# Optimization experiments

Hardware: AMD Instinct MI355X
Metric: run time of the kernel (lower is better)

The kernel has to match this reference:

```python
import jax, jax.numpy as jnp
import numpy as np

# Scaled-up constants (GRID_SIZE=96)
AFFINE_HIDDEN_DIM = 128
ATTENTION_DIM = 256
EMBEDDING_DIM = 512
MAX_CONTRAST = 1.8
RANGE_SIZE = 4
NUM_RANGE_BLOCKS = 13824   # (96//4)**3
NUM_DOMAIN_BLOCKS = 1728   # (96//8)**3
SOFTMAX_TEMPERATURE = 0.25


def setup_inputs() -> dict:
    key = jax.random.key(0)
    ks = jax.random.split(key, 17)
    E, A, H = EMBEDDING_DIM, ATTENTION_DIM, AFFINE_HIDDEN_DIM
    NR, ND = NUM_RANGE_BLOCKS, NUM_DOMAIN_BLOCKS
    s_lin = 1.0 / np.sqrt(E)  # torch Linear default init scale
    return {
        "pooled_domains": jax.random.normal(ks[0], (ND, RANGE_SIZE, RANGE_SIZE, RANGE_SIZE), jnp.float32),
        "range_latents": jax.random.normal(ks[1], (NR, E), jnp.float32),
        "domain_latents": jax.random.normal(ks[2], (ND, E), jnp.float32),
        "range_positional": jax.random.normal(ks[3], (NR, E), jnp.float32),
        "domain_positional": jax.random.normal(ks[4], (ND, E), jnp.float32),
        "W_rproj": jax.random.normal(ks[5], (E, A), jnp.float32) * s_lin,
        "b_rproj": jax.random.normal(ks[6], (A,), jnp.float32) * s_lin,
        "W_dproj": jax.random.normal(ks[7], (E, A), jnp.float32) * s_lin,
        "b_dproj": jax.random.normal(ks[8], (A,), jnp.float32) * s_lin,
        "W_rcon": jax.random.normal(ks[9], (E, H), jnp.float32) * s_lin,
        "b_rcon": jax.random.normal(ks[10], (H,), jnp.float32) * s_lin,
        "W_dcon": jax.random.normal(ks[11], (E, H), jnp.float32) * s_lin,
        "b_dcon": jax.random.normal(ks[12], (H,), jnp.float32) * s_lin,
        "W_roff": jax.random.normal(ks[13], (E, H), jnp.float32) * s_lin,
        "b_roff": jax.random.normal(ks[14], (H,), jnp.float32) * s_lin,
        "W_doff": jax.random.normal(ks[15], (E, H), jnp.float32) * s_lin,
        "b_doff": jax.random.normal(ks[16], (H,), jnp.float32) * s_lin,
    }


def reference(pooled_domains, range_latents, domain_latents,
              range_positional, domain_positional,
              W_rproj, b_rproj, W_dproj, b_dproj,
              W_rcon, b_rcon, W_dcon, b_dcon,
              W_roff, b_roff, W_doff, b_doff):
    range_base = range_latents + range_positional      # [NR, E]
    domain_base = domain_latents + domain_positional   # [ND, E]

    range_repr = range_base @ W_rproj + b_rproj        # [NR, A]
    domain_repr = domain_base @ W_dproj + b_dproj      # [ND, A]

    inv_sqrt_h = 1.0 / np.sqrt(AFFINE_HIDDEN_DIM).astype(np.float32)
    range_con = range_base @ W_rcon + b_rcon           # [NR, H]
    domain_con = domain_base @ W_dcon + b_dcon         # [ND, H]
    contrast = jnp.tanh((range_con @ domain_con.T) * inv_sqrt_h) * MAX_CONTRAST  # [NR, ND]

    range_off = range_base @ W_roff + b_roff
    domain_off = domain_base @ W_doff + b_doff
    offset = jnp.tanh((range_off @ domain_off.T) * inv_sqrt_h)  # [NR, ND]

    scale = 1.0 / (np.sqrt(ATTENTION_DIM).astype(np.float32) * SOFTMAX_TEMPERATURE)
    logits = (range_repr @ domain_repr.T) * scale      # [NR, ND]
    weights = jax.nn.softmax(logits, axis=-1)          # [NR, ND]

    domain_flat = pooled_domains.reshape(NUM_DOMAIN_BLOCKS, -1)   # [ND, 64]
    scaled_domains = (weights * contrast) @ domain_flat           # [NR, 64]
    offset_effective = jnp.sum(weights * offset, axis=1, keepdims=True)  # [NR, 1]
    decoded = (scaled_domains + offset_effective).reshape(-1, RANGE_SIZE, RANGE_SIZE, RANGE_SIZE)
    return decoded
```

## Files before the change

kernel.cpp:

```cpp
#include <hip/hip_runtime.h>
#include <stdint.h>

#define NRB 13824
#define NDB 1728
#define EDIM 512
#define SPLIT 18
#define DPB (NDB/SPLIT)
#define TILES (DPB/32)

typedef __attribute__((ext_vector_type(8))) _Float16 h8;
typedef __attribute__((ext_vector_type(4))) float f4;
typedef __attribute__((ext_vector_type(4))) unsigned short us4;

typedef __attribute__((address_space(3))) void lds_void;
typedef const __attribute__((address_space(1))) void gbl_void;

#define MFMA(a,b,c) __builtin_amdgcn_mfma_f32_16x16x32_f16(a,b,c,0,0,0)

static __device__ __forceinline__ ushort f2h(float f){
  union { _Float16 h; ushort u; } cv;
  cv.h = (_Float16)f;
  return cv.u;
}

static __device__ __forceinline__ float tanh_fast(float x){
  float ax = __builtin_fabsf(x);
  float t = __builtin_amdgcn_exp2f(ax * -2.8853900817779268f);
  float r = (1.0f - t) * __builtin_amdgcn_rcpf(1.0f + t);
  return __builtin_copysignf(r, x);
}

__global__ void prep_kernel(
    const float* __restrict__ pooled,
    const float* __restrict__ rlat, const float* __restrict__ dlat,
    const float* __restrict__ rpos, const float* __restrict__ dpos,
    const float* __restrict__ Wrp, const float* __restrict__ brp,
    const float* __restrict__ Wdp, const float* __restrict__ bdp,
    const float* __restrict__ Wrc, const float* __restrict__ brc,
    const float* __restrict__ Wdc, const float* __restrict__ bdc,
    const float* __restrict__ Wro, const float* __restrict__ bro,
    const float* __restrict__ Wdo2, const float* __restrict__ bdo2,
    ushort* __restrict__ rb, ushort* __restrict__ db,
    ushort* __restrict__ Wr_t, ushort* __restrict__ Wd_t,
    float* __restrict__ br_c, float* __restrict__ bd_c,
    ushort* __restrict__ dflt)
{
  const int NRE = NRB*EDIM, NDE = NDB*EDIM;
  int i0 = blockIdx.x*blockDim.x + threadIdx.x;
  int stride = gridDim.x*blockDim.x;
  for (int i=i0; i<NRE; i+=stride) rb[i] = f2h(rlat[i]+rpos[i]);
  for (int i=i0; i<NDE; i+=stride) db[i] = f2h(dlat[i]+dpos[i]);
  for (int i=i0; i<512*512; i+=stride){
    int n = i>>9, k = i&511;
    float vr = (n<256) ? Wrp[k*256+n] : ((n<384) ? Wrc[k*128+(n-256)] : Wro[k*128+(n-384)]);
    float vd = (n<256) ? Wdp[k*256+n] : ((n<384) ? Wdc[k*128+(n-256)] : Wdo2[k*128+(n-384)]);
    Wr_t[i] = f2h(vr); Wd_t[i] = f2h(vd);
  }
  for (int i=i0; i<512; i+=stride){
    br_c[i] = (i<256) ? brp[i] : ((i<384) ? brc[i-256] : bro[i-384]);
    bd_c[i] = (i<256) ? bdp[i] : ((i<384) ? bdc[i-256] : bdo2[i-384]);
  }
  for (int i=i0; i<64*NDB; i+=stride){
    int c = i/NDB, d = i - c*NDB;
    dflt[i] = f2h(pooled[d*64+c]);
  }
}

__global__ __launch_bounds__(256) void gemm_feats(
    const ushort* __restrict__ A,
    const ushort* __restrict__ Bt,
    const float* __restrict__ bias,
    ushort* __restrict__ C,
    int M)
{
  __shared__ ushort As[128*32];
  __shared__ ushort Bs[128*32];
  const int tid = threadIdx.x;
  const int lane = tid & 63;
  const int wave = tid >> 6;
  const int l15 = lane & 15;
  const int lhi = lane >> 4;
  const int row0 = blockIdx.x * 128;
  const int col0 = blockIdx.y * 128;
  const int wr = (wave>>1)*64;
  const int wc = (wave&1)*64;

  f4 acc[4][4] = {};
  char* Ab = (char*)As; char* Bb = (char*)Bs;

  for (int k0=0; k0<EDIM; k0+=32){
    __syncthreads();
    #pragma unroll
    for (int c=0;c<2;c++){
      int L = (tid + c*256)*16;
      int r = L>>6;
      int kb = L&63;
      int kbs = kb ^ ((r&3)<<4);
      int ra = row0 + r; if (ra > M-1) ra = M-1;
      const ushort* srcA = A + (size_t)ra*EDIM + k0 + (kbs>>1);
      const ushort* srcB = Bt + (size_t)(col0+r)*EDIM + k0 + (kbs>>1);
      __builtin_amdgcn_global_load_lds((gbl_void*)srcA, (lds_void*)(Ab + L), 16, 0, 0);
      __builtin_amdgcn_global_load_lds((gbl_void*)srcB, (lds_void*)(Bb + L), 16, 0, 0);
    }
    __syncthreads();
    h8 af[4], bf[4];
    #pragma unroll
    for (int i=0;i<4;i++){
      int rowa = wr + i*16 + l15;
      af[i] = *(const h8*)(Ab + (((rowa*64) + lhi*16) ^ ((rowa&3)<<4)));
      int rowb = wc + i*16 + l15;
      bf[i] = *(const h8*)(Bb + (((rowb*64) + lhi*16) ^ ((rowb&3)<<4)));
    }
    #pragma unroll
    for (int i=0;i<4;i++){
      #pragma unroll
      for (int j=0;j<4;j++){
        acc[i][j] = MFMA(af[i], bf[j], acc[i][j]);
      }
    }
  }

  #pragma unroll
  for (int j=0;j<4;j++){
    int col = col0 + wc + j*16 + l15;
    float bv = bias[col];
    #pragma unroll
    for (int i=0;i<4;i++){
      #pragma unroll
      for (int r=0;r<4;r++){
        int row = row0 + wr + i*16 + lhi*4 + r;
        if (row < M) C[(size_t)row*EDIM + col] = f2h(acc[i][j][r] + bv);
      }
    }
  }
}

__global__ __launch_bounds__(512, 2) void attn_kernel(
    const ushort* __restrict__ rfeat,
    const ushort* __restrict__ dfeat,
    const ushort* __restrict__ dflt,
    ushort* __restrict__ accbuf,
    float* __restrict__ mlbuf)
{
  __shared__ ushort DF[DPB*512];
  __shared__ ushort PT[8][16*32];

  const int tid  = threadIdx.x;
  const int wave = tid >> 6;
  const int lane = tid & 63;
  const int l15  = lane & 15;
  const int lhi  = lane >> 4;
  const int wrow = blockIdx.x*128 + wave*16;
  const int by   = blockIdx.y;
  const int dbase = by * DPB;

  constexpr float CL = 0.25f * 1.4426950408889634f;
  constexpr float CH = 0.08838834764831845f;

  char* DFb = (char*)DF;
  char* PTb = (char*)PT[wave];

  #pragma unroll
  for (int c=0;c<12;c++){
    int id = tid + c*512;
    int dom = id >> 6;
    h8 v = *(const h8*)(dfeat + (size_t)(dbase+dom)*EDIM + (id&63)*8);
    *(h8*)(DFb + ((id*16) ^ ((dom&7)<<4))) = v;
  }

  h8 q[16];
  {
    const ushort* qr = rfeat + (size_t)(wrow + l15)*EDIM + lhi*8;
    #pragma unroll
    for (int c=0;c<16;c++) q[c] = *(const h8*)(qr + c*32);
  }

  f4 acc[4] = {};
  float m = -1e30f, lsum = 0.f, offa = 0.f;
  const int sb = (lane & 48) + ((lane >> 4) << 2);

  __syncthreads();

  for (int t=0; t<TILES; ++t){
    const int d0 = dbase + t*32;
    const int dloc = t*32;

    f4 SL[2] = {}, SC[2] = {}, SO[2] = {};
    #pragma unroll
    for (int ct=0; ct<2; ++ct){
      const int dom = dloc + ct*16 + l15;
      const int swz = (dom&7)<<4;
      const int base = dom*1024 + lhi*16;
      #pragma unroll
      for (int c=0;c<8;c++){
        h8 b = *(const h8*)(DFb + ((base + c*64) ^ swz));
        SL[ct] = MFMA(b, q[c], SL[ct]);
      }
      #pragma unroll
      for (int c=8;c<12;c++){
        h8 b = *(const h8*)(DFb + ((base + c*64) ^ swz));
        SC[ct] = MFMA(b, q[c], SC[ct]);
      }
      #pragma unroll
      for (int c=12;c<16;c++){
        h8 b = *(const h8*)(DFb + ((base + c*64) ^ swz));
        SO[ct] = MFMA(b, q[c], SO[ct]);
      }
    }

    float lm = fmaxf(
        fmaxf(fmaxf(SL[0][0],SL[0][1]), fmaxf(SL[0][2],SL[0][3])),
        fmaxf(fmaxf(SL[1][0],SL[1][1]), fmaxf(SL[1][2],SL[1][3]))) * CL;
    lm = fmaxf(lm, __shfl_xor(lm, 16, 64));
    lm = fmaxf(lm, __shfl_xor(lm, 32, 64));
    float mn = fmaxf(m, lm);
    float al = __builtin_amdgcn_exp2f(m - mn);
    m = mn;
    lsum *= al; offa *= al;

    us4 w0, w1;
    #pragma unroll
    for (int r=0;r<4;r++){
      float p0 = __builtin_amdgcn_exp2f(SL[0][r]*CL - mn);
      float p1 = __builtin_amdgcn_exp2f(SL[1][r]*CL - mn);
      lsum += p0 + p1;
      float c0 = tanh_fast(SC[0][r]*CH)*1.8f;
      float c1 = tanh_fast(SC[1][r]*CH)*1.8f;
      float o0 = tanh_fast(SO[0][r]*CH);
      float o1 = tanh_fast(SO[1][r]*CH);
      offa += p0*o0 + p1*o1;
      w0[r] = f2h(p0*c0);
      w1[r] = f2h(p1*c1);
    }
    {
      const int wbase = l15*64;
      const int xs = (l15&3)<<4;
      *(us4*)(PTb + ((wbase + lhi*8) ^ xs))      = w0;
      *(us4*)(PTb + ((wbase + 32 + lhi*8) ^ xs)) = w1;
    }

    __builtin_amdgcn_sched_barrier(0);

    {
      float alr[4];
      #pragma unroll
      for (int r=0;r<4;r++) alr[r] = __shfl(al, sb + r, 64);
      #pragma unroll
      for (int nt=0; nt<4; nt++){
        acc[nt][0]*=alr[0]; acc[nt][1]*=alr[1];
        acc[nt][2]*=alr[2]; acc[nt][3]*=alr[3];
      }
      h8 pa = *(const h8*)(PTb + ((l15*64 + lhi*16) ^ ((l15&3)<<4)));
      #pragma unroll
      for (int nt=0; nt<4; nt++){
        int n = nt*16 + l15;
        h8 vb = *(const h8*)(dflt + (size_t)n*NDB + d0 + lhi*8);
        acc[nt] = MFMA(pa, vb, acc[nt]);
      }
    }

    __builtin_amdgcn_sched_barrier(0);
  }

  float ls = lsum, oa = offa;
  ls += __shfl_xor(ls, 16, 64); ls += __shfl_xor(ls, 32, 64);
  oa += __shfl_xor(oa, 16, 64); oa += __shfl_xor(oa, 32, 64);

  #pragma unroll
  for (int r=0;r<4;r++){
    int row = wrow + lhi*4 + r;
    size_t base = ((size_t)by*NRB + row)*64;
    #pragma unroll
    for (int nt=0; nt<4; nt++){
      accbuf[base + nt*16 + l15] = f2h(acc[nt][r]);
    }
  }
  if (lane < 16){
    size_t mo = ((size_t)by*NRB + wrow + l15)*4;
    mlbuf[mo+0] = m;
    mlbuf[mo+1] = ls;
    mlbuf[mo+2] = oa;
  }
}

__global__ __launch_bounds__(256) void combine_kernel(
    const ushort* __restrict__ accbuf,
    const float* __restrict__ mlbuf,
    float* __restrict__ out)
{
  __shared__ float wS[64][SPLIT];
  __shared__ float c0S[64], iTS[64];
  const int rb = blockIdx.x;
  const int tid = threadIdx.x;

  if (tid < 64){
    int row = rb*64 + tid;
    float M = -1e30f;
    float m[SPLIT], l[SPLIT], o[SPLIT];
    #pragma unroll
    for (int s=0;s<SPLIT;s++){
      size_t off = ((size_t)s*NRB + row)*4;
      m[s]=mlbuf[off]; l[s]=mlbuf[off+1]; o[s]=mlbuf[off+2];
      M = fmaxf(M, m[s]);
    }
    float T=0.f, C=0.f;
    #pragma unroll
    for (int s=0;s<SPLIT;s++){
      float w = __builtin_amdgcn_exp2f(m[s]-M);
      wS[tid][s]=w; T += l[s]*w; C += o[s]*w;
    }
    c0S[tid]=C; iTS[tid]=1.0f/T;
  }
  __syncthreads();

  const int row_l = tid>>2;
  const int cb = (tid&3)*16;
  const int row = rb*64 + row_l;
  float res[16] = {};
  #pragma unroll
  for (int s=0;s<SPLIT;s++){
    float w = wS[row_l][s];
    const ushort* ap = accbuf + ((size_t)s*NRB + row)*64 + cb;
    h8 v0 = *(const h8*)(ap);
    h8 v1 = *(const h8*)(ap + 8);
    #pragma unroll
    for (int j=0;j<8;j++){
      res[j]   += (float)v0[j]*w;
      res[j+8] += (float)v1[j]*w;
    }
  }
  float C = c0S[row_l], iT = iTS[row_l];
  #pragma unroll
  for (int j=0;j<16;j++) out[(size_t)row*64 + cb + j] = (res[j]+C)*iT;
}

extern "C" void kernel_launch(void* const* d_in, const int* in_sizes, int n_in,
                              void* d_out, int out_size, void* d_ws, size_t ws_size,
                              hipStream_t stream) {
  const float* pooled = (const float*)d_in[0];
  const float* rlat   = (const float*)d_in[1];
  const float* dlat   = (const float*)d_in[2];
  const float* rpos   = (const float*)d_in[3];
  const float* dpos   = (const float*)d_in[4];
  const float* Wrp    = (const float*)d_in[5];
  const float* brp    = (const float*)d_in[6];
  const float* Wdp    = (const float*)d_in[7];
  const float* bdp    = (const float*)d_in[8];
  const float* Wrc    = (const float*)d_in[9];
  const float* brc    = (const float*)d_in[10];
  const float* Wdc    = (const float*)d_in[11];
  const float* bdc    = (const float*)d_in[12];
  const float* Wro    = (const float*)d_in[13];
  const float* bro    = (const float*)d_in[14];
  const float* Wdo2   = (const float*)d_in[15];
  const float* bdo2   = (const float*)d_in[16];

  char* ws = (char*)d_ws;
  size_t off = 0;
  ushort* rb    = (ushort*)(ws + off); off += (size_t)NRB*EDIM*2;
  ushort* db    = (ushort*)(ws + off); off += (size_t)NDB*EDIM*2;
  ushort* Wr_t  = (ushort*)(ws + off); off += (size_t)512*512*2;
  ushort* Wd_t  = (ushort*)(ws + off); off += (size_t)512*512*2;
  float*  br_c  = (float*)(ws + off);  off += 512*4;
  float*  bd_c  = (float*)(ws + off);  off += 512*4;
  ushort* rfeat = (ushort*)(ws + off); off += (size_t)NRB*EDIM*2;
  ushort* dfeat = (ushort*)(ws + off); off += (size_t)NDB*EDIM*2;
  ushort* dflt  = (ushort*)(ws + off); off += (size_t)64*NDB*2;
  ushort* accb  = (ushort*)(ws + off); off += (size_t)SPLIT*NRB*64*2;
  float*  mlb   = (float*)(ws + off);  off += (size_t)SPLIT*NRB*4*4;

  prep_kernel<<<2048, 256, 0, stream>>>(pooled, rlat, dlat, rpos, dpos,
      Wrp, brp, Wdp, bdp, Wrc, brc, Wdc, bdc, Wro, bro, Wdo2, bdo2,
      rb, db, Wr_t, Wd_t, br_c, bd_c, dflt);

  gemm_feats<<<dim3(108,4), 256, 0, stream>>>(rb, Wr_t, br_c, rfeat, NRB);
  gemm_feats<<<dim3(14,4),  256, 0, stream>>>(db, Wd_t, bd_c, dfeat, NDB);

  attn_kernel<<<dim3(108, SPLIT), 512, 0, stream>>>(rfeat, dfeat, dflt, accb, mlb);
  combine_kernel<<<216, 256, 0, stream>>>(accb, mlb, (float*)d_out);
}
```

Baseline: 150.6 us.

## Process two query row-groups per wave to reuse LDS domain tiles

Each wave now handles two 16-row query groups (256 rows per block) instead of one, so every domain-feature fragment read from LDS and every dflt global load feeds two sets of MFMAs. The grid is halved in x, which halves the per-block LDS fill of domain features overall. The cost is double the query registers (32 h8) and accumulators per wave, which under launch_bounds(512,2) may cause spills or lower occupancy, and only 972 blocks remain to spread across the CUs.

```diff
diff --git a/kernel.cpp b/kernel.cpp
--- a/kernel.cpp
+++ b/kernel.cpp
@@ -143,22 +143,22 @@
     float* __restrict__ mlbuf)
 {
   __shared__ ushort DF[DPB*512];
-  __shared__ ushort PT[8][16*32];
+  __shared__ ushort PT[8][2][16*32];
 
   const int tid  = threadIdx.x;
   const int wave = tid >> 6;
   const int lane = tid & 63;
   const int l15  = lane & 15;
   const int lhi  = lane >> 4;
-  const int wrow = blockIdx.x*128 + wave*16;
   const int by   = blockIdx.y;
   const int dbase = by * DPB;
+  const int wrow0 = blockIdx.x*256 + wave*16;
+  const int wrow1 = wrow0 + 128;
 
   constexpr float CL = 0.25f * 1.4426950408889634f;
   constexpr float CH = 0.08838834764831845f;
 
   char* DFb = (char*)DF;
-  char* PTb = (char*)PT[wave];
 
   #pragma unroll
   for (int c=0;c<12;c++){
@@ -168,15 +168,16 @@
     *(h8*)(DFb + ((id*16) ^ ((dom&7)<<4))) = v;
   }
 
-  h8 q[16];
-  {
-    const ushort* qr = rfeat + (size_t)(wrow + l15)*EDIM + lhi*8;
-    #pragma unroll
-    for (int c=0;c<16;c++) q[c] = *(const h8*)(qr + c*32);
-  }
-
-  f4 acc[4] = {};
-  float m = -1e30f, lsum = 0.f, offa = 0.f;
+  h8 q[2][16];
+  #pragma unroll
+  for (int g=0; g<2; g++){
+    const ushort* qr = rfeat + (size_t)((g ? wrow1 : wrow0) + l15)*EDIM + lhi*8;
+    #pragma unroll
+    for (int c=0;c<16;c++) q[g][c] = *(const h8*)(qr + c*32);
+  }
+
+  f4 acc[2][4] = {};
+  float m[2] = {-1e30f, -1e30f}, lsum[2] = {0.f,0.f}, offa[2] = {0.f,0.f};
   const int sb = (lane & 48) + ((lane >> 4) << 2);
 
   __syncthreads();
@@ -185,101 +186,120 @@
     const int d0 = dbase + t*32;
     const int dloc = t*32;
 
-    f4 SL[2] = {}, SC[2] = {}, SO[2] = {};
-    #pragma unroll
-    for (int ct=0; ct<2; ++ct){
-      const int dom = dloc + ct*16 + l15;
-      const int swz = (dom&7)<<4;
-      const int base = dom*1024 + lhi*16;
-      #pragma unroll
-      for (int c=0;c<8;c++){
-        h8 b = *(const h8*)(DFb + ((base + c*64) ^ swz));
-        SL[ct] = MFMA(b, q[c], SL[ct]);
-      }
-      #pragma unroll
-      for (int c=8;c<12;c++){
-        h8 b = *(const h8*)(DFb + ((base + c*64) ^ swz));
-        SC[ct] = MFMA(b, q[c], SC[ct]);
-      }
-      #pragma unroll
-      for (int c=12;c<16;c++){
-        h8 b = *(const h8*)(DFb + ((base + c*64) ^ swz));
-        SO[ct] = MFMA(b, q[c], SO[ct]);
-      }
-    }
-
-    float lm = fmaxf(
-        fmaxf(fmaxf(SL[0][0],SL[0][1]), fmaxf(SL[0][2],SL[0][3])),
-        fmaxf(fmaxf(SL[1][0],SL[1][1]), fmaxf(SL[1][2],SL[1][3]))) * CL;
-    lm = fmaxf(lm, __shfl_xor(lm, 16, 64));
-    lm = fmaxf(lm, __shfl_xor(lm, 32, 64));
-    float mn = fmaxf(m, lm);
-    float al = __builtin_amdgcn_exp2f(m - mn);
-    m = mn;
-    lsum *= al; offa *= al;
-
-    us4 w0, w1;
+    h8 vb[4];
+    #pragma unroll
+    for (int nt=0; nt<4; nt++){
+      int n = nt*16 + l15;
+      vb[nt] = *(const h8*)(dflt + (size_t)n*NDB + d0 + lhi*8);
+    }
+
+    float al2[2];
+
+    #pragma unroll
+    for (int g=0; g<2; g++){
+      char* PTb = (char*)PT[wave][g];
+
+      f4 SL[2] = {}, SC[2] = {}, SO[2] = {};
+      #pragma unroll
+      for (int ct=0; ct<2; ++ct){
+        const int dom = dloc + ct*16 + l15;
+        const int swz = (dom&7)<<4;
+        const int base = dom*1024 + lhi*16;
+        #pragma unroll
+        for (int c=0;c<8;c++){
+          h8 b = *(const h8*)(DFb + ((base + c*64) ^ swz));
+          SL[ct] = MFMA(b, q[g][c], SL[ct]);
+        }
+        #pragma unroll
+        for (int c=8;c<12;c++){
+          h8 b = *(const h8*)(DFb + ((base + c*64) ^ swz));
+          SC[ct] = MFMA(b, q[g][c], SC[ct]);
+        }
+        #pragma unroll
+        for (int c=12;c<16;c++){
+          h8 b = *(const h8*)(DFb + ((base + c*64) ^ swz));
+          SO[ct] = MFMA(b, q[g][c], SO[ct]);
+        }
+      }
+
+      float lm = fmaxf(
+          fmaxf(fmaxf(SL[0][0],SL[0][1]), fmaxf(SL[0][2],SL[0][3])),
+          fmaxf(fmaxf(SL[1][0],SL[1][1]), fmaxf(SL[1][2],SL[1][3]))) * CL;
+      lm = fmaxf(lm, __shfl_xor(lm, 16, 64));
+      lm = fmaxf(lm, __shfl_xor(lm, 32, 64));
+      float mn = fmaxf(m[g], lm);
+      float al = __builtin_amdgcn_exp2f(m[g] - mn);
+      m[g] = mn;
+      lsum[g] *= al; offa[g] *= al;
+      al2[g] = al;
+
+      us4 w0, w1;
+      #pragma unroll
+      for (int r=0;r<4;r++){
+        float p0 = __builtin_amdgcn_exp2f(SL[0][r]*CL - mn);
+        float p1 = __builtin_amdgcn_exp2f(SL[1][r]*CL - mn);
+        lsum[g] += p0 + p1;
+        float c0 = tanh_fast(SC[0][r]*CH)*1.8f;
+        float c1 = tanh_fast(SC[1][r]*CH)*1.8f;
+        float o0 = tanh_fast(SO[0][r]*CH);
+        float o1 = tanh_fast(SO[1][r]*CH);
+        offa[g] += p0*o0 + p1*o1;
+        w0[r] = f2h(p0*c0);
+        w1[r] = f2h(p1*c1);
+      }
+      {
+        const int wbase = l15*64;
+        const int xs = (l15&3)<<4;
+        *(us4*)(PTb + ((wbase + lhi*8) ^ xs))      = w0;
+        *(us4*)(PTb + ((wbase + 32 + lhi*8) ^ xs)) = w1;
+      }
+    }
+
+    __builtin_amdgcn_sched_barrier(0);
+
+    #pragma unroll
+    for (int g=0; g<2; g++){
+      char* PTb = (char*)PT[wave][g];
+      float alr[4];
+      #pragma unroll
+      for (int r=0;r<4;r++) alr[r] = __shfl(al2[g], sb + r, 64);
+      #pragma unroll
+      for (int nt=0; nt<4; nt++){
+        acc[g][nt][0]*=alr[0]; acc[g][nt][1]*=alr[1];
+        acc[g][nt][2]*=alr[2]; acc[g][nt][3]*=alr[3];
+      }
+      h8 pa = *(const h8*)(PTb + ((l15*64 + lhi*16) ^ ((l15&3)<<4)));
+      #pragma unroll
+      for (int nt=0; nt<4; nt++){
+        acc[g][nt] = MFMA(pa, vb[nt], acc[g][nt]);
+      }
+    }
+
+    __builtin_amdgcn_sched_barrier(0);
+  }
+
+  #pragma unroll
+  for (int g=0; g<2; g++){
+    const int wrow = g ? wrow1 : wrow0;
+    float ls = lsum[g], oa = offa[g];
+    ls += __shfl_xor(ls, 16, 64); ls += __shfl_xor(ls, 32, 64);
+    oa += __shfl_xor(oa, 16, 64); oa += __shfl_xor(oa, 32, 64);
+
     #pragma unroll
     for (int r=0;r<4;r++){
-      float p0 = __builtin_amdgcn_exp2f(SL[0][r]*CL - mn);
-      float p1 = __builtin_amdgcn_exp2f(SL[1][r]*CL - mn);
-      lsum += p0 + p1;
-      float c0 = tanh_fast(SC[0][r]*CH)*1.8f;
-      float c1 = tanh_fast(SC[1][r]*CH)*1.8f;
-      float o0 = tanh_fast(SO[0][r]*CH);
-      float o1 = tanh_fast(SO[1][r]*CH);
-      offa += p0*o0 + p1*o1;
-      w0[r] = f2h(p0*c0);
-      w1[r] = f2h(p1*c1);
-    }
-    {
-      const int wbase = l15*64;
-      const int xs = (l15&3)<<4;
-      *(us4*)(PTb + ((wbase + lhi*8) ^ xs))      = w0;
-      *(us4*)(PTb + ((wbase + 32 + lhi*8) ^ xs)) = w1;
-    }
-
-    __builtin_amdgcn_sched_barrier(0);
-
-    {
-      float alr[4];
-      #pragma unroll
-      for (int r=0;r<4;r++) alr[r] = __shfl(al, sb + r, 64);
+      int row = wrow + lhi*4 + r;
+      size_t base = ((size_t)by*NRB + row)*64;
       #pragma unroll
       for (int nt=0; nt<4; nt++){
-        acc[nt][0]*=alr[0]; acc[nt][1]*=alr[1];
-        acc[nt][2]*=alr[2]; acc[nt][3]*=alr[3];
-      }
-      h8 pa = *(const h8*)(PTb + ((l15*64 + lhi*16) ^ ((l15&3)<<4)));
-      #pragma unroll
-      for (int nt=0; nt<4; nt++){
-        int n = nt*16 + l15;
-        h8 vb = *(const h8*)(dflt + (size_t)n*NDB + d0 + lhi*8);
-        acc[nt] = MFMA(pa, vb, acc[nt]);
-      }
-    }
-
-    __builtin_amdgcn_sched_barrier(0);
-  }
-
-  float ls = lsum, oa = offa;
-  ls += __shfl_xor(ls, 16, 64); ls += __shfl_xor(ls, 32, 64);
-  oa += __shfl_xor(oa, 16, 64); oa += __shfl_xor(oa, 32, 64);
-
-  #pragma unroll
-  for (int r=0;r<4;r++){
-    int row = wrow + lhi*4 + r;
-    size_t base = ((size_t)by*NRB + row)*64;
-    #pragma unroll
-    for (int nt=0; nt<4; nt++){
-      accbuf[base + nt*16 + l15] = f2h(acc[nt][r]);
-    }
-  }
-  if (lane < 16){
-    size_t mo = ((size_t)by*NRB + wrow + l15)*4;
-    mlbuf[mo+0] = m;
-    mlbuf[mo+1] = ls;
-    mlbuf[mo+2] = oa;
+        accbuf[base + nt*16 + l15] = f2h(acc[g][nt][r]);
+      }
+    }
+    if (lane < 16){
+      size_t mo = ((size_t)by*NRB + wrow + l15)*4;
+      mlbuf[mo+0] = m[g];
+      mlbuf[mo+1] = ls;
+      mlbuf[mo+2] = oa;
+    }
   }
 }
 
@@ -376,6 +396,6 @@
   gemm_feats<<<dim3(108,4), 256, 0, stream>>>(rb, Wr_t, br_c, rfeat, NRB);
   gemm_feats<<<dim3(14,4),  256, 0, stream>>>(db, Wd_t, bd_c, dfeat, NDB);
 
-  attn_kernel<<<dim3(108, SPLIT), 512, 0, stream>>>(rfeat, dfeat, dflt, accb, mlb);
+  attn_kernel<<<dim3(54, SPLIT), 512, 0, stream>>>(rfeat, dfeat, dflt, accb, mlb);
   combine_kernel<<<216, 256, 0, stream>>>(accb, mlb, (float*)d_out);
 }
```

Result: slower. 175.4 us (+16.5%).
